# Kernel optimization log

Hardware: AMD Instinct MI355X
Metric: run time of the kernel (lower is better)

## Reference

```python
import jax, jax.numpy as jnp
import numpy as np

N_NODES = 50000
N_EDGES = 640000
N_GRAPHS = 256
H = 128
L = 4
X_DIM, P_DIM, E_DIM = 64, 16, 16


def setup_inputs() -> dict:
    key = jax.random.key(0)
    ks = jax.random.split(key, 16)
    s = 0.05
    inp = {
        "x": jax.random.normal(ks[0], (N_NODES, X_DIM), jnp.float32),
        "p": jax.random.normal(ks[1], (N_NODES, P_DIM), jnp.float32),
        "e_attr": jax.random.normal(ks[2], (N_EDGES, E_DIM), jnp.float32),
        "edge_index": jax.random.randint(ks[3], (2, N_EDGES), 0, N_NODES, jnp.int32),
        "batch": jnp.sort(jax.random.randint(ks[4], (N_NODES,), 0, N_GRAPHS, jnp.int32)),
        # embeddings
        "W_embed": jax.random.normal(ks[5], (X_DIM + P_DIM, H), jnp.float32) * s,
        "b_embed": jnp.zeros((H,), jnp.float32),
        "W_eembed": jax.random.normal(ks[6], (E_DIM, H), jnp.float32) * s,
        "b_eembed": jnp.zeros((H,), jnp.float32),
        # per-layer stacked params
        "Wm": jax.random.normal(ks[7], (L, 3 * H, H), jnp.float32) * s,
        "bm": jnp.zeros((L, H), jnp.float32),
        "Wh": jax.random.normal(ks[8], (L, 2 * H, H), jnp.float32) * s,
        "bh": jnp.zeros((L, H), jnp.float32),
        "We": jax.random.normal(ks[9], (L, 3 * H, H), jnp.float32) * s,
        "be": jnp.zeros((L, H), jnp.float32),
    }
    return inp


def reference(x, p, e_attr, W_embed, b_embed, W_eembed, b_eembed,
              Wm, bm, Wh, bh, We, be, edge_index, batch):
    # node embed: Linear(cat(x, p))
    h = jnp.concatenate([x, p], axis=1) @ W_embed + b_embed          # [N, H]
    e = e_attr @ W_eembed + b_eembed                                 # [E, H]
    send, rec = edge_index[0], edge_index[1]
    n_nodes = x.shape[0]
    for l in range(Wm.shape[0]):
        h_send, h_rec = h[send], h[rec]                              # gathers [E, H]
        cat_ser = jnp.concatenate([h_send, h_rec, e], axis=1)        # [E, 3H]
        messages = cat_ser @ Wm[l] + bm[l]                           # [E, H]
        messages_agg = jax.ops.segment_sum(messages, rec, num_segments=n_nodes)  # scatter_add
        h = jnp.concatenate([h, messages_agg], axis=1) @ Wh[l] + bh[l]
        # e_update uses h_send/h_rec gathered from the PRE-update h (as in torch code)
        e = cat_ser @ We[l] + be[l]
    # global_add_pool over graphs
    out = jax.ops.segment_sum(h, batch, num_segments=N_GRAPHS)       # [G, H]
    return out
```

## Files before the change

### kernel.cpp

```cpp
#include <hip/hip_runtime.h>
#include <cstdio>

#define NN 50000
#define NE 640000
#define NG 256
#define NL 4

#define SCAN_CHUNK 1024
#define NB_SCAN ((NN + SCAN_CHUNK - 1) / SCAN_CHUNK)

typedef unsigned short u16;
typedef unsigned int u32;
typedef __attribute__((ext_vector_type(8))) short short8v;
typedef __attribute__((ext_vector_type(4))) float f32x4;

static __device__ __forceinline__ float bf2f(u16 v) {
    return __uint_as_float(((u32)v) << 16);
}
static __device__ __forceinline__ u16 f2bf(float f) {
    u32 u = __float_as_uint(f);
    u += 0x7fff + ((u >> 16) & 1);
    return (u16)(u >> 16);
}

__global__ __launch_bounds__(256) void k_deg(
    const int* __restrict__ rec, int* __restrict__ deg)
{
    const int e = blockIdx.x * 256 + threadIdx.x;
    atomicAdd(&deg[rec[e]], 1);
}

__global__ __launch_bounds__(256) void k_prep_xp(
    const float* __restrict__ x, const float* __restrict__ p,
    u16* __restrict__ Axp)
{
    const int idx = blockIdx.x * 256 + threadIdx.x;
    const int row = idx / 48;
    const int c2 = idx - row * 48;
    const int c0 = c2 * 2;
    float f0, f1;
    if (c0 < 64)      { f0 = x[(size_t)row * 64 + c0]; f1 = x[(size_t)row * 64 + c0 + 1]; }
    else if (c0 < 80) { f0 = p[(size_t)row * 16 + c0 - 64]; f1 = p[(size_t)row * 16 + c0 - 63]; }
    else              { f0 = 0.f; f1 = 0.f; }
    ((u32*)Axp)[idx] = (u32)f2bf(f0) | ((u32)f2bf(f1) << 16);
}

__global__ __launch_bounds__(256) void k_wembed(
    const float* __restrict__ W, u16* __restrict__ Wp)
{
    const int idx = blockIdx.x * 256 + threadIdx.x;
    const int ks = idx >> 12;
    const int rem = idx & 4095;
    const int col = rem >> 5;
    const int kk = rem & 31;
    const int k = ks * 32 + kk;
    Wp[((size_t)ks * 128 + col) * 32 + kk] = f2bf(k < 80 ? W[k * 128 + col] : 0.f);
}

__global__ __launch_bounds__(256) void k_embed(
    const u16* __restrict__ Axp, const u16* __restrict__ Wp,
    const float* __restrict__ b, const int* __restrict__ deg,
    u16* __restrict__ h, u16* __restrict__ dh)
{
    const int t = threadIdx.x;
    const int lane = t & 63;
    const int w = t >> 6;
    const int rb = blockIdx.x * 128 + w * 32;
    const int l15 = lane & 15;
    const int kg  = lane >> 4;

    int r0 = rb + l15;      if (r0 > NN - 1) r0 = NN - 1;
    int r1 = rb + 16 + l15; if (r1 > NN - 1) r1 = NN - 1;

    f32x4 acc[2][8];
    #pragma unroll
    for (int m = 0; m < 2; ++m)
        #pragma unroll
        for (int n = 0; n < 8; ++n) acc[m][n] = (f32x4){0.f, 0.f, 0.f, 0.f};

    #pragma unroll
    for (int ks = 0; ks < 3; ++ks) {
        const short8v a0 = *(const short8v*)(Axp + (size_t)r0 * 96 + ks * 32 + kg * 8);
        const short8v a1 = *(const short8v*)(Axp + (size_t)r1 * 96 + ks * 32 + kg * 8);
        const u16* bb = Wp + ((size_t)ks * 128 + l15) * 32 + kg * 8;
        #pragma unroll
        for (int nf = 0; nf < 8; ++nf) {
            const short8v bv = *(const short8v*)(bb + (size_t)nf * 16 * 32);
            acc[0][nf] = __builtin_amdgcn_mfma_f32_16x16x32_bf16(a0, bv, acc[0][nf], 0, 0, 0);
            acc[1][nf] = __builtin_amdgcn_mfma_f32_16x16x32_bf16(a1, bv, acc[1][nf], 0, 0, 0);
        }
    }

    #pragma unroll
    for (int m = 0; m < 2; ++m) {
        #pragma unroll
        for (int r = 0; r < 4; ++r) {
            const int row = rb + m * 16 + kg * 4 + r;
            if (row < NN) {
                const float dg = (float)deg[row];
                #pragma unroll
                for (int nf = 0; nf < 8; ++nf) {
                    const int col = nf * 16 + l15;
                    const float v = acc[m][nf][r] + b[col];
                    h[(size_t)row * 128 + col]  = f2bf(v);
                    dh[(size_t)row * 128 + col] = f2bf(bf2f(f2bf(v)) * dg);
                }
            }
        }
    }
}

__global__ __launch_bounds__(256) void k_wprep(
    const float* __restrict__ Wm, const float* __restrict__ Wh,
    const float* __restrict__ We, const float* __restrict__ bm,
    float* __restrict__ Wb, float* __restrict__ cvec)
{
    const int idx = blockIdx.x * 256 + threadIdx.x;
    const int total = 4 * 512 * 256;
    if (idx < total) {
        const int l = idx >> 17;
        const int rem = idx & 131071;
        const int k = rem >> 8;
        const int c = rem & 255;
        const float* Wm_l = Wm + (size_t)l * 384 * 128;
        const float* Wh_l = Wh + (size_t)l * 256 * 128;
        const float* We_l = We + (size_t)l * 384 * 128;
        float v;
        if (k < 128) {
            v = (c < 128) ? Wh_l[k * 128 + c] : 0.f;
        } else {
            const int kk  = (k - 128) & 127;
            const int blk = (k - 128) >> 7;
            const int roff = (blk == 0) ? 128 : (blk == 1) ? 0 : 256;
            if (c < 128) {
                float s = 0.f;
                #pragma unroll 4
                for (int j = 0; j < 128; ++j)
                    s += Wm_l[(roff + kk) * 128 + j] * Wh_l[(128 + j) * 128 + c];
                v = s;
            } else {
                v = We_l[(roff + kk) * 128 + (c - 128)];
            }
        }
        Wb[idx] = v;
    } else if (idx < total + 512) {
        const int r = idx - total;
        const int l = r >> 7;
        const int c = r & 127;
        const float* Wh_l = Wh + (size_t)l * 256 * 128;
        const float* bm_l = bm + l * 128;
        float s = 0.f;
        #pragma unroll 4
        for (int j = 0; j < 128; ++j) s += bm_l[j] * Wh_l[(128 + j) * 128 + c];
        cvec[r] = s;
    }
}

__global__ __launch_bounds__(256) void k_wswz(
    const float* __restrict__ Wb, u16* __restrict__ Bp)
{
    const int idx = blockIdx.x * 256 + threadIdx.x;
    const int l = idx >> 17;
    const int rem = idx & 131071;
    const int k = rem >> 8;
    const int n = rem & 255;
    Bp[(((size_t)l * 16 + (k >> 5)) * 256 + n) * 32 + (k & 31)] = f2bf(Wb[idx]);
}

__global__ __launch_bounds__(256) void k_scanA(
    const int* __restrict__ deg, int* __restrict__ part)
{
    __shared__ int red[256];
    const int t = threadIdx.x;
    const int base = blockIdx.x * SCAN_CHUNK + t * 4;
    int s = 0;
    #pragma unroll
    for (int i = 0; i < 4; ++i) {
        const int idx = base + i;
        if (idx < NN) s += deg[idx];
    }
    red[t] = s;
    __syncthreads();
    for (int off = 128; off > 0; off >>= 1) {
        if (t < off) red[t] += red[t + off];
        __syncthreads();
    }
    if (t == 0) part[blockIdx.x] = red[0];
}

__global__ __launch_bounds__(64) void k_scanB(int* part)
{
    if (threadIdx.x == 0) {
        int run = 0;
        for (int b = 0; b < NB_SCAN; ++b) {
            const int v = part[b];
            part[b] = run;
            run += v;
        }
    }
}

__global__ __launch_bounds__(256) void k_scanC(
    const int* __restrict__ deg, const int* __restrict__ part,
    int* __restrict__ offs, int* __restrict__ cursor)
{
    __shared__ int ts[256];
    const int t = threadIdx.x;
    const int base = blockIdx.x * SCAN_CHUNK + t * 4;
    int v[4]; int s = 0;
    #pragma unroll
    for (int i = 0; i < 4; ++i) {
        const int idx = base + i;
        v[i] = (idx < NN) ? deg[idx] : 0;
        s += v[i];
    }
    ts[t] = s;
    __syncthreads();
    for (int off = 1; off < 256; off <<= 1) {
        int val = ts[t];
        if (t >= off) val += ts[t - off];
        __syncthreads();
        ts[t] = val;
        __syncthreads();
    }
    int run = part[blockIdx.x] + ((t == 0) ? 0 : ts[t - 1]);
    #pragma unroll
    for (int i = 0; i < 4; ++i) {
        const int idx = base + i;
        if (idx < NN) { offs[idx] = run; cursor[idx] = run; run += v[i]; }
    }
}

__global__ __launch_bounds__(256) void k_fill(
    const int* __restrict__ send, const int* __restrict__ rec,
    int* __restrict__ cursor, int* __restrict__ csr, int* __restrict__ csr_e)
{
    const int e = blockIdx.x * 256 + threadIdx.x;
    const int r = rec[e];
    const int pos = atomicAdd(&cursor[r], 1);
    csr[pos] = send[e];
    csr_e[pos] = e;
}

__global__ __launch_bounds__(256) void k_sea_se0(
    const float* __restrict__ ea, const int* __restrict__ csr_e,
    const int* __restrict__ offs, const int* __restrict__ deg,
    const float* __restrict__ Wee, const float* __restrict__ bee,
    u16* __restrict__ Se)
{
    __shared__ float sea[4][16];
    const int t = threadIdx.x;
    const int lane = t & 63;
    const int w = t >> 6;
    const int nb = blockIdx.x * 4;
    const int node = nb + w;
    const int g = lane >> 4;
    const int l16 = lane & 15;
    const int off = offs[node];
    const int d = deg[node];

    float acc = 0.f;
    for (int j = 0; j < d; j += 4) {
        const int jj = j + g;
        if (jj < d) {
            const int eid = csr_e[off + jj];
            acc += ea[(size_t)eid * 16 + l16];
        }
    }
    acc += __shfl_xor(acc, 16);
    acc += __shfl_xor(acc, 32);
    if (g == 0) sea[w][l16] = acc;
    __syncthreads();

    const int c = t & 127;
    #pragma unroll
    for (int q = 0; q < 2; ++q) {
        const int n = (t >> 7) + 2 * q;
        const int nd = nb + n;
        float a = (float)deg[nd] * bee[c];
        #pragma unroll
        for (int k = 0; k < 16; ++k) a += sea[n][k] * Wee[k * 128 + c];
        Se[(size_t)nd * 128 + c] = f2bf(a);
    }
}

__global__ __launch_bounds__(256) void k_gather(
    const u16* __restrict__ h, const int* __restrict__ csr,
    const int* __restrict__ offs, const int* __restrict__ deg,
    u16* __restrict__ Sh)
{
    const int t = threadIdx.x;
    const int lane = t & 63;
    const int node = blockIdx.x * 4 + (t >> 6);
    const int g = lane >> 4;
    const int l16 = lane & 15;
    const int off = offs[node];
    const int d = deg[node];
    const uint4* hp = (const uint4*)h;

    float acc[8];
    #pragma unroll
    for (int i = 0; i < 8; ++i) acc[i] = 0.f;

    for (int j = 0; j < d; j += 4) {
        const int jj = j + g;
        if (jj < d) {
            const int s = csr[off + jj];
            const uint4 v = hp[(size_t)s * 16 + l16];
            acc[0] += bf2f((u16)(v.x & 0xffff)); acc[1] += bf2f((u16)(v.x >> 16));
            acc[2] += bf2f((u16)(v.y & 0xffff)); acc[3] += bf2f((u16)(v.y >> 16));
            acc[4] += bf2f((u16)(v.z & 0xffff)); acc[5] += bf2f((u16)(v.z >> 16));
            acc[6] += bf2f((u16)(v.w & 0xffff)); acc[7] += bf2f((u16)(v.w >> 16));
        }
    }
    #pragma unroll
    for (int i = 0; i < 8; ++i) {
        float s = acc[i];
        s += __shfl_xor(s, 16);
        s += __shfl_xor(s, 32);
        acc[i] = s;
    }
    if (g == 0) {
        uint4 o;
        o.x = (u32)f2bf(acc[0]) | ((u32)f2bf(acc[1]) << 16);
        o.y = (u32)f2bf(acc[2]) | ((u32)f2bf(acc[3]) << 16);
        o.z = (u32)f2bf(acc[4]) | ((u32)f2bf(acc[5]) << 16);
        o.w = (u32)f2bf(acc[6]) | ((u32)f2bf(acc[7]) << 16);
        ((uint4*)Sh)[(size_t)node * 16 + l16] = o;
    }
}

template<bool FULL>
__global__ __launch_bounds__(256) void k_dense(
    const u16* __restrict__ h, const u16* __restrict__ dh,
    const u16* __restrict__ Sh, const u16* __restrict__ Se,
    const int* __restrict__ deg, const u16* __restrict__ Bp,
    const float* __restrict__ cvec, const float* __restrict__ bh,
    const float* __restrict__ be,
    u16* __restrict__ h_out, u16* __restrict__ dh_out, u16* __restrict__ Se_out)
{
    const int t = threadIdx.x;
    const int lane = t & 63;
    const int w = t >> 6;
    const int wm = w & 1;
    const int wn = w >> 1;
    if (!FULL && wn == 1) return;
    const int rb = blockIdx.x * 64 + wm * 32;
    const int cb = wn * 128;
    const int l15 = lane & 15;
    const int kg  = lane >> 4;

    int r0 = rb + l15;      if (r0 > NN - 1) r0 = NN - 1;
    int r1 = rb + 16 + l15; if (r1 > NN - 1) r1 = NN - 1;
    const size_t a0off = (size_t)r0 * 128 + kg * 8;
    const size_t a1off = (size_t)r1 * 128 + kg * 8;

    f32x4 acc[2][8];
    #pragma unroll
    for (int m = 0; m < 2; ++m)
        #pragma unroll
        for (int n = 0; n < 8; ++n) acc[m][n] = (f32x4){0.f, 0.f, 0.f, 0.f};

    #pragma unroll
    for (int s = 0; s < 4; ++s) {
        const u16* __restrict__ Sp = (s == 0) ? h : (s == 1) ? dh : (s == 2) ? Sh : Se;
        #pragma unroll
        for (int k4 = 0; k4 < 4; ++k4) {
            const int ks = s * 4 + k4;
            const short8v a0 = *(const short8v*)(Sp + a0off + k4 * 32);
            const short8v a1 = *(const short8v*)(Sp + a1off + k4 * 32);
            const u16* bb = Bp + (((size_t)ks * 256) + cb + l15) * 32 + kg * 8;
            #pragma unroll
            for (int nf = 0; nf < 8; ++nf) {
                const short8v b = *(const short8v*)(bb + (size_t)nf * 16 * 32);
                acc[0][nf] = __builtin_amdgcn_mfma_f32_16x16x32_bf16(a0, b, acc[0][nf], 0, 0, 0);
                acc[1][nf] = __builtin_amdgcn_mfma_f32_16x16x32_bf16(a1, b, acc[1][nf], 0, 0, 0);
            }
        }
    }

    #pragma unroll
    for (int m = 0; m < 2; ++m) {
        #pragma unroll
        for (int r = 0; r < 4; ++r) {
            const int row = rb + m * 16 + kg * 4 + r;
            if (row < NN) {
                const float dg = (float)deg[row];
                if (cb == 0) {
                    #pragma unroll
                    for (int nf = 0; nf < 8; ++nf) {
                        const int col = nf * 16 + l15;
                        const float v = acc[m][nf][r] + bh[col] + dg * cvec[col];
                        h_out[(size_t)row * 128 + col] = f2bf(v);
                        if (FULL)
                            dh_out[(size_t)row * 128 + col] = f2bf(bf2f(f2bf(v)) * dg);
                    }
                } else {
                    #pragma unroll
                    for (int nf = 0; nf < 8; ++nf) {
                        const int col = nf * 16 + l15;
                        const float v = acc[m][nf][r] + dg * be[col];
                        Se_out[(size_t)row * 128 + col] = f2bf(v);
                    }
                }
            }
        }
    }
}

__global__ __launch_bounds__(256) void k_pool(
    const u16* __restrict__ h, const int* __restrict__ batch,
    float* __restrict__ out)
{
    const int t = threadIdx.x;
    const int col = t & 127;
    const int half = t >> 7;
    const int base = blockIdx.x * 64 + half * 32;
    float acc = 0.f;
    int curg = -1;
    for (int i = 0; i < 32; ++i) {
        const int n = base + i;
        if (n >= NN) break;
        const int g = batch[n];
        if (g != curg) {
            if (curg >= 0) atomicAdd(&out[curg * 128 + col], acc);
            curg = g; acc = 0.f;
        }
        acc += bf2f(h[(size_t)n * 128 + col]);
    }
    if (curg >= 0) atomicAdd(&out[curg * 128 + col], acc);
}

extern "C" void kernel_launch(void* const* d_in, const int* in_sizes, int n_in,
                              void* d_out, int out_size, void* d_ws, size_t ws_size,
                              hipStream_t stream)
{
    const float* x       = (const float*)d_in[0];
    const float* p       = (const float*)d_in[1];
    const float* ea      = (const float*)d_in[2];
    const int*   eidx    = (const int*)d_in[3];
    const int*   batch   = (const int*)d_in[4];
    const float* W_embed = (const float*)d_in[5];
    const float* b_embed = (const float*)d_in[6];
    const float* W_ee    = (const float*)d_in[7];
    const float* b_ee    = (const float*)d_in[8];
    const float* Wm      = (const float*)d_in[9];
    const float* bm      = (const float*)d_in[10];
    const float* Wh      = (const float*)d_in[11];
    const float* bh      = (const float*)d_in[12];
    const float* We      = (const float*)d_in[13];
    const float* be      = (const float*)d_in[14];
    const int* send = eidx;
    const int* rec  = eidx + NE;

    char* w = (char*)d_ws;
    const size_t NHb = (size_t)NN * 128 * sizeof(u16);
    u16* hA  = (u16*)w; w += NHb;
    u16* hB  = (u16*)w; w += NHb;
    u16* dhA = (u16*)w; w += NHb;
    u16* dhB = (u16*)w; w += NHb;
    u16* SeA = (u16*)w; w += NHb;
    u16* SeB = (u16*)w; w += NHb;
    u16* Sh  = (u16*)w; w += NHb;
    u16* Axp = (u16*)w;  w += (size_t)NN * 96 * 2;
    int*  deg    = (int*)w;   w += (size_t)NN * 4;
    int*  offs   = (int*)w;   w += (size_t)(NN + 4) * 4;
    int*  cursor = (int*)w;   w += (size_t)NN * 4;
    int*  csr    = (int*)w;   w += (size_t)NE * 4;
    int*  csr_e  = (int*)w;   w += (size_t)NE * 4;
    int*  part   = (int*)w;   w += 64 * 4;
    float* Wb    = (float*)w; w += (size_t)4 * 512 * 256 * 4;
    float* cvec  = (float*)w; w += 512 * 4;
    u16*  Bp     = (u16*)w;   w += (size_t)4 * 512 * 256 * 2;
    u16*  Wpe    = (u16*)w;   w += (size_t)3 * 128 * 32 * 2;
    const size_t need = (size_t)(w - (char*)d_ws);
    if (ws_size < need) {
        fprintf(stderr, "[kernel_launch] ws_size=%zu < needed=%zu — skipping\n",
                ws_size, need);
        return;
    }

    float* out = (float*)d_out;

    hipMemsetAsync(d_out, 0, (size_t)NG * 128 * sizeof(float), stream);
    hipMemsetAsync(deg, 0, (size_t)NN * sizeof(int), stream);

    k_deg<<<NE / 256, 256, 0, stream>>>(rec, deg);
    k_prep_xp<<<NN * 48 / 256, 256, 0, stream>>>(x, p, Axp);
    k_wembed<<<3 * 128 * 32 / 256, 256, 0, stream>>>(W_embed, Wpe);
    k_embed<<<(NN + 127) / 128, 256, 0, stream>>>(Axp, Wpe, b_embed, deg, hA, dhA);
    k_wprep<<<(4 * 512 * 256 + 512 + 255) / 256, 256, 0, stream>>>(Wm, Wh, We, bm, Wb, cvec);
    k_wswz<<<4 * 512 * 256 / 256, 256, 0, stream>>>(Wb, Bp);
    k_scanA<<<NB_SCAN, 256, 0, stream>>>(deg, part);
    k_scanB<<<1, 64, 0, stream>>>(part);
    k_scanC<<<NB_SCAN, 256, 0, stream>>>(deg, part, offs, cursor);
    k_fill<<<NE / 256, 256, 0, stream>>>(send, rec, cursor, csr, csr_e);
    k_sea_se0<<<NN / 4, 256, 0, stream>>>(ea, csr_e, offs, deg, W_ee, b_ee, SeA);

    u16* h_cur = hA;   u16* h_nxt = hB;
    u16* dh_cur = dhA; u16* dh_nxt = dhB;
    u16* Se_cur = SeA; u16* Se_nxt = SeB;
    for (int l = 0; l < NL; ++l) {
        k_gather<<<NN / 4, 256, 0, stream>>>(h_cur, csr, offs, deg, Sh);
        if (l < NL - 1)
            k_dense<true><<<(NN + 63) / 64, 256, 0, stream>>>(h_cur, dh_cur, Sh, Se_cur,
                deg, Bp + (size_t)l * 512 * 256,
                cvec + l * 128, bh + l * 128, be + l * 128,
                h_nxt, dh_nxt, Se_nxt);
        else
            k_dense<false><<<(NN + 63) / 64, 256, 0, stream>>>(h_cur, dh_cur, Sh, Se_cur,
                deg, Bp + (size_t)l * 512 * 256,
                cvec + l * 128, bh + l * 128, be + l * 128,
                h_nxt, dh_nxt, Se_nxt);
        u16* tmp;
        tmp = h_cur;  h_cur  = h_nxt;  h_nxt  = tmp;
        tmp = dh_cur; dh_cur = dh_nxt; dh_nxt = tmp;
        tmp = Se_cur; Se_cur = Se_nxt; Se_nxt = tmp;
    }
    k_pool<<<(NN + 63) / 64, 256, 0, stream>>>(h_cur, batch, out);
}
```

Baseline: 520.9 us.

## Fuse neighbor gather into dense layer kernel and compute degree-scaled h on the fly

Merges the per-layer gather kernel into the dense GEMM kernel. Each block sums neighbor h rows for its 64 nodes into shared memory, then runs the MFMA GEMM reading the aggregate from LDS. The separately stored dh = deg*h buffer is removed and recomputed in registers from h and deg, which cuts global writes and reads per layer and drops one launch per layer. The cost is that the irregular gather now runs inside the GEMM kernel, one wave per 16 nodes in sequence, with fewer waves in flight to hide gather latency, plus extra per-element conversion work for the scaling.

```diff
diff --git a/kernel.cpp b/kernel.cpp
--- a/kernel.cpp
+++ b/kernel.cpp
@@ -21,6 +21,15 @@
     u32 u = __float_as_uint(f);
     u += 0x7fff + ((u >> 16) & 1);
     return (u16)(u >> 16);
+}
+static __device__ __forceinline__ short8v scale8(short8v a, float s) {
+    short8v r;
+    #pragma unroll
+    for (int i = 0; i < 8; ++i) {
+        const float f = bf2f((u16)a[i]) * s;
+        r[i] = (short)f2bf(f);
+    }
+    return r;
 }
 
 __global__ __launch_bounds__(256) void k_deg(
@@ -59,8 +68,7 @@
 
 __global__ __launch_bounds__(256) void k_embed(
     const u16* __restrict__ Axp, const u16* __restrict__ Wp,
-    const float* __restrict__ b, const int* __restrict__ deg,
-    u16* __restrict__ h, u16* __restrict__ dh)
+    const float* __restrict__ b, u16* __restrict__ h)
 {
     const int t = threadIdx.x;
     const int lane = t & 63;
@@ -97,13 +105,10 @@
         for (int r = 0; r < 4; ++r) {
             const int row = rb + m * 16 + kg * 4 + r;
             if (row < NN) {
-                const float dg = (float)deg[row];
                 #pragma unroll
                 for (int nf = 0; nf < 8; ++nf) {
                     const int col = nf * 16 + l15;
-                    const float v = acc[m][nf][r] + b[col];
-                    h[(size_t)row * 128 + col]  = f2bf(v);
-                    dh[(size_t)row * 128 + col] = f2bf(bf2f(f2bf(v)) * dg);
+                    h[(size_t)row * 128 + col] = f2bf(acc[m][nf][r] + b[col]);
                 }
             }
         }
@@ -260,12 +265,9 @@
     const int d = deg[node];
 
     float acc = 0.f;
-    for (int j = 0; j < d; j += 4) {
-        const int jj = j + g;
-        if (jj < d) {
-            const int eid = csr_e[off + jj];
-            acc += ea[(size_t)eid * 16 + l16];
-        }
+    for (int j = g; j < d; j += 4) {
+        const int eid = csr_e[off + j];
+        acc += ea[(size_t)eid * 16 + l16];
     }
     acc += __shfl_xor(acc, 16);
     acc += __shfl_xor(acc, 32);
@@ -284,76 +286,72 @@
     }
 }
 
-__global__ __launch_bounds__(256) void k_gather(
-    const u16* __restrict__ h, const int* __restrict__ csr,
-    const int* __restrict__ offs, const int* __restrict__ deg,
-    u16* __restrict__ Sh)
-{
-    const int t = threadIdx.x;
-    const int lane = t & 63;
-    const int node = blockIdx.x * 4 + (t >> 6);
-    const int g = lane >> 4;
-    const int l16 = lane & 15;
-    const int off = offs[node];
-    const int d = deg[node];
-    const uint4* hp = (const uint4*)h;
-
-    float acc[8];
-    #pragma unroll
-    for (int i = 0; i < 8; ++i) acc[i] = 0.f;
-
-    for (int j = 0; j < d; j += 4) {
-        const int jj = j + g;
-        if (jj < d) {
-            const int s = csr[off + jj];
-            const uint4 v = hp[(size_t)s * 16 + l16];
-            acc[0] += bf2f((u16)(v.x & 0xffff)); acc[1] += bf2f((u16)(v.x >> 16));
-            acc[2] += bf2f((u16)(v.y & 0xffff)); acc[3] += bf2f((u16)(v.y >> 16));
-            acc[4] += bf2f((u16)(v.z & 0xffff)); acc[5] += bf2f((u16)(v.z >> 16));
-            acc[6] += bf2f((u16)(v.w & 0xffff)); acc[7] += bf2f((u16)(v.w >> 16));
-        }
-    }
-    #pragma unroll
-    for (int i = 0; i < 8; ++i) {
-        float s = acc[i];
-        s += __shfl_xor(s, 16);
-        s += __shfl_xor(s, 32);
-        acc[i] = s;
-    }
-    if (g == 0) {
-        uint4 o;
-        o.x = (u32)f2bf(acc[0]) | ((u32)f2bf(acc[1]) << 16);
-        o.y = (u32)f2bf(acc[2]) | ((u32)f2bf(acc[3]) << 16);
-        o.z = (u32)f2bf(acc[4]) | ((u32)f2bf(acc[5]) << 16);
-        o.w = (u32)f2bf(acc[6]) | ((u32)f2bf(acc[7]) << 16);
-        ((uint4*)Sh)[(size_t)node * 16 + l16] = o;
-    }
-}
-
 template<bool FULL>
-__global__ __launch_bounds__(256) void k_dense(
-    const u16* __restrict__ h, const u16* __restrict__ dh,
-    const u16* __restrict__ Sh, const u16* __restrict__ Se,
-    const int* __restrict__ deg, const u16* __restrict__ Bp,
+__global__ __launch_bounds__(256) void k_layer(
+    const u16* __restrict__ h, const u16* __restrict__ Se,
+    const int* __restrict__ deg, const int* __restrict__ offs,
+    const int* __restrict__ csr, const u16* __restrict__ Bp,
     const float* __restrict__ cvec, const float* __restrict__ bh,
     const float* __restrict__ be,
-    u16* __restrict__ h_out, u16* __restrict__ dh_out, u16* __restrict__ Se_out)
-{
+    u16* __restrict__ h_out, u16* __restrict__ Se_out)
+{
+    __shared__ u16 ShT[64 * 136];
     const int t = threadIdx.x;
     const int lane = t & 63;
     const int w = t >> 6;
+    const int n0 = blockIdx.x * 64;
+
+    {
+        const int g = lane >> 4;
+        const int l16 = lane & 15;
+        const uint4* hp = (const uint4*)h;
+        for (int i = 0; i < 16; ++i) {
+            const int node = n0 + w * 16 + i;
+            float a[8];
+            #pragma unroll
+            for (int q = 0; q < 8; ++q) a[q] = 0.f;
+            if (node < NN) {
+                const int off = offs[node];
+                const int d = deg[node];
+                for (int j = g; j < d; j += 4) {
+                    const uint4 v = hp[(size_t)csr[off + j] * 16 + l16];
+                    a[0] += bf2f((u16)(v.x & 0xffff)); a[1] += bf2f((u16)(v.x >> 16));
+                    a[2] += bf2f((u16)(v.y & 0xffff)); a[3] += bf2f((u16)(v.y >> 16));
+                    a[4] += bf2f((u16)(v.z & 0xffff)); a[5] += bf2f((u16)(v.z >> 16));
+                    a[6] += bf2f((u16)(v.w & 0xffff)); a[7] += bf2f((u16)(v.w >> 16));
+                }
+            }
+            #pragma unroll
+            for (int q = 0; q < 8; ++q) {
+                a[q] += __shfl_xor(a[q], 16);
+                a[q] += __shfl_xor(a[q], 32);
+            }
+            if (g == 0) {
+                uint4 o;
+                o.x = (u32)f2bf(a[0]) | ((u32)f2bf(a[1]) << 16);
+                o.y = (u32)f2bf(a[2]) | ((u32)f2bf(a[3]) << 16);
+                o.z = (u32)f2bf(a[4]) | ((u32)f2bf(a[5]) << 16);
+                o.w = (u32)f2bf(a[6]) | ((u32)f2bf(a[7]) << 16);
+                *(uint4*)&ShT[(w * 16 + i) * 136 + l16 * 8] = o;
+            }
+        }
+    }
+    __syncthreads();
+
     const int wm = w & 1;
     const int wn = w >> 1;
     if (!FULL && wn == 1) return;
-    const int rb = blockIdx.x * 64 + wm * 32;
+    const int rb = n0 + wm * 32;
     const int cb = wn * 128;
     const int l15 = lane & 15;
     const int kg  = lane >> 4;
 
     int r0 = rb + l15;      if (r0 > NN - 1) r0 = NN - 1;
     int r1 = rb + 16 + l15; if (r1 > NN - 1) r1 = NN - 1;
-    const size_t a0off = (size_t)r0 * 128 + kg * 8;
-    const size_t a1off = (size_t)r1 * 128 + kg * 8;
+    const float dga0 = (float)deg[r0];
+    const float dga1 = (float)deg[r1];
+    const int lr0 = wm * 32 + l15;
+    const int lr1 = wm * 32 + 16 + l15;
 
     f32x4 acc[2][8];
     #pragma unroll
@@ -362,13 +360,22 @@
         for (int n = 0; n < 8; ++n) acc[m][n] = (f32x4){0.f, 0.f, 0.f, 0.f};
 
     #pragma unroll
-    for (int s = 0; s < 4; ++s) {
-        const u16* __restrict__ Sp = (s == 0) ? h : (s == 1) ? dh : (s == 2) ? Sh : Se;
-        #pragma unroll
-        for (int k4 = 0; k4 < 4; ++k4) {
+    for (int k4 = 0; k4 < 4; ++k4) {
+        const int ko = k4 * 32 + kg * 8;
+        const short8v ah0 = *(const short8v*)(h + (size_t)r0 * 128 + ko);
+        const short8v ah1 = *(const short8v*)(h + (size_t)r1 * 128 + ko);
+        const short8v ad0 = scale8(ah0, dga0);
+        const short8v ad1 = scale8(ah1, dga1);
+        const short8v as0 = *(const short8v*)&ShT[lr0 * 136 + ko];
+        const short8v as1 = *(const short8v*)&ShT[lr1 * 136 + ko];
+        const short8v ae0 = *(const short8v*)(Se + (size_t)r0 * 128 + ko);
+        const short8v ae1 = *(const short8v*)(Se + (size_t)r1 * 128 + ko);
+
+        #pragma unroll
+        for (int s = 0; s < 4; ++s) {
+            const short8v a0 = (s == 0) ? ah0 : (s == 1) ? ad0 : (s == 2) ? as0 : ae0;
+            const short8v a1 = (s == 0) ? ah1 : (s == 1) ? ad1 : (s == 2) ? as1 : ae1;
             const int ks = s * 4 + k4;
-            const short8v a0 = *(const short8v*)(Sp + a0off + k4 * 32);
-            const short8v a1 = *(const short8v*)(Sp + a1off + k4 * 32);
             const u16* bb = Bp + (((size_t)ks * 256) + cb + l15) * 32 + kg * 8;
             #pragma unroll
             for (int nf = 0; nf < 8; ++nf) {
@@ -390,17 +397,15 @@
                     #pragma unroll
                     for (int nf = 0; nf < 8; ++nf) {
                         const int col = nf * 16 + l15;
-                        const float v = acc[m][nf][r] + bh[col] + dg * cvec[col];
-                        h_out[(size_t)row * 128 + col] = f2bf(v);
-                        if (FULL)
-                            dh_out[(size_t)row * 128 + col] = f2bf(bf2f(f2bf(v)) * dg);
+                        h_out[(size_t)row * 128 + col] =
+                            f2bf(acc[m][nf][r] + bh[col] + dg * cvec[col]);
                     }
                 } else {
                     #pragma unroll
                     for (int nf = 0; nf < 8; ++nf) {
                         const int col = nf * 16 + l15;
-                        const float v = acc[m][nf][r] + dg * be[col];
-                        Se_out[(size_t)row * 128 + col] = f2bf(v);
+                        Se_out[(size_t)row * 128 + col] =
+                            f2bf(acc[m][nf][r] + dg * be[col]);
                     }
                 }
             }
@@ -457,11 +462,8 @@
     const size_t NHb = (size_t)NN * 128 * sizeof(u16);
     u16* hA  = (u16*)w; w += NHb;
     u16* hB  = (u16*)w; w += NHb;
-    u16* dhA = (u16*)w; w += NHb;
-    u16* dhB = (u16*)w; w += NHb;
     u16* SeA = (u16*)w; w += NHb;
     u16* SeB = (u16*)w; w += NHb;
-    u16* Sh  = (u16*)w; w += NHb;
     u16* Axp = (u16*)w;  w += (size_t)NN * 96 * 2;
     int*  deg    = (int*)w;   w += (size_t)NN * 4;
     int*  offs   = (int*)w;   w += (size_t)(NN + 4) * 4;
@@ -488,7 +490,7 @@
     k_deg<<<NE / 256, 256, 0, stream>>>(rec, deg);
     k_prep_xp<<<NN * 48 / 256, 256, 0, stream>>>(x, p, Axp);
     k_wembed<<<3 * 128 * 32 / 256, 256, 0, stream>>>(W_embed, Wpe);
-    k_embed<<<(NN + 127) / 128, 256, 0, stream>>>(Axp, Wpe, b_embed, deg, hA, dhA);
+    k_embed<<<(NN + 127) / 128, 256, 0, stream>>>(Axp, Wpe, b_embed, hA);
     k_wprep<<<(4 * 512 * 256 + 512 + 255) / 256, 256, 0, stream>>>(Wm, Wh, We, bm, Wb, cvec);
     k_wswz<<<4 * 512 * 256 / 256, 256, 0, stream>>>(Wb, Bp);
     k_scanA<<<NB_SCAN, 256, 0, stream>>>(deg, part);
@@ -498,23 +500,18 @@
     k_sea_se0<<<NN / 4, 256, 0, stream>>>(ea, csr_e, offs, deg, W_ee, b_ee, SeA);
 
     u16* h_cur = hA;   u16* h_nxt = hB;
-    u16* dh_cur = dhA; u16* dh_nxt = dhB;
     u16* Se_cur = SeA; u16* Se_nxt = SeB;
     for (int l = 0; l < NL; ++l) {
-        k_gather<<<NN / 4, 256, 0, stream>>>(h_cur, csr, offs, deg, Sh);
         if (l < NL - 1)
-            k_dense<true><<<(NN + 63) / 64, 256, 0, stream>>>(h_cur, dh_cur, Sh, Se_cur,
-                deg, Bp + (size_t)l * 512 * 256,
-                cvec + l * 128, bh + l * 128, be + l * 128,
-                h_nxt, dh_nxt, Se_nxt);
+            k_layer<true><<<(NN + 63) / 64, 256, 0, stream>>>(h_cur, Se_cur,
+                deg, offs, csr, Bp + (size_t)l * 512 * 256,
+                cvec + l * 128, bh + l * 128, be + l * 128, h_nxt, Se_nxt);
         else
-            k_dense<false><<<(NN + 63) / 64, 256, 0, stream>>>(h_cur, dh_cur, Sh, Se_cur,
-                deg, Bp + (size_t)l * 512 * 256,
-                cvec + l * 128, bh + l * 128, be + l * 128,
-                h_nxt, dh_nxt, Se_nxt);
+            k_layer<false><<<(NN + 63) / 64, 256, 0, stream>>>(h_cur, Se_cur,
+                deg, offs, csr, Bp + (size_t)l * 512 * 256,
+                cvec + l * 128, bh + l * 128, be + l * 128, h_nxt, Se_nxt);
         u16* tmp;
         tmp = h_cur;  h_cur  = h_nxt;  h_nxt  = tmp;
-        tmp = dh_cur; dh_cur = dh_nxt; dh_nxt = tmp;
         tmp = Se_cur; Se_cur = Se_nxt; Se_nxt = tmp;
     }
     k_pool<<<(NN + 63) / 64, 256, 0, stream>>>(h_cur, batch, out);
```

New measurement: 698.1 us. 1.34x slower.
